# Kernel optimization log

Measured on AMD Instinct MI355X. Metric: run time of the kernel, lower is better.

Reference implementation:

```python
import jax, jax.numpy as jnp
import numpy as np

IMG_W, IMG_H = 800, 800
OH, OW = 7, 7


def setup_inputs() -> dict:
    key = jax.random.key(0)
    k1, k2, k3 = jax.random.split(key, 3)
    feature_map = jax.random.normal(k1, (1, 256, 200, 200), dtype=jnp.float32)
    # boxes in image pixel coords, x1<=x2 and y1<=y2
    xs = jnp.sort(jax.random.uniform(k2, (1024, 2), dtype=jnp.float32) * (IMG_W - 1), axis=1)
    ys = jnp.sort(jax.random.uniform(k3, (1024, 2), dtype=jnp.float32) * (IMG_H - 1), axis=1)
    boxes = jnp.stack([xs[:, 0], ys[:, 0], xs[:, 1], ys[:, 1]], axis=1)
    return {"feature_map": feature_map, "boxes": boxes}


def reference(feature_map, boxes):
    # feature_map: [1, C, H, W]; boxes: [N, 4] (x1, y1, x2, y2) in image coords
    fm = feature_map[0]                      # [C, H, W]
    C, H, W = fm.shape
    scale = jnp.array([W / IMG_W, H / IMG_H, W / IMG_W, H / IMG_H], dtype=boxes.dtype)
    b = jnp.floor(boxes * scale).astype(jnp.int32)
    x1 = jnp.clip(b[:, 0], 0, W - 1)
    y1 = jnp.clip(b[:, 1], 0, H - 1)
    x2 = jnp.clip(b[:, 2] + 1, x1 + 1, W)    # exclusive end, clamped like torch slicing
    y2 = jnp.clip(b[:, 3] + 1, y1 + 1, H)
    rh = y2 - y1                             # [N]
    rw = x2 - x1
    # adaptive_avg_pool2d bin edges: start=floor(i*L/O), end=ceil((i+1)*L/O)
    i = jnp.arange(OH)
    j = jnp.arange(OW)
    rs = y1[:, None] + (i[None, :] * rh[:, None]) // OH                  # [N, OH]
    re = y1[:, None] + ((i[None, :] + 1) * rh[:, None] + OH - 1) // OH
    cs = x1[:, None] + (j[None, :] * rw[:, None]) // OW                  # [N, OW]
    ce = x1[:, None] + ((j[None, :] + 1) * rw[:, None] + OW - 1) // OW
    # integral image with zero row/col padding: ii[c, r, k] = sum fm[c, :r, :k]
    ii = jnp.pad(jnp.cumsum(jnp.cumsum(fm, axis=1), axis=2), ((0, 0), (1, 0), (1, 0)))

    def S(r, c):  # r: [N, OH], c: [N, OW] -> [N, C, OH, OW]
        return ii[:, r[:, :, None], c[:, None, :]].transpose(1, 0, 2, 3)

    total = S(re, ce) - S(rs, ce) - S(re, cs) + S(rs, cs)               # [N, C, OH, OW]
    area = ((re - rs)[:, :, None] * (ce - cs)[:, None, :]).astype(fm.dtype)  # [N, OH, OW]
    return total / area[:, None, :, :]
```

## Files before the change

### kernel.cpp

```cpp
#include <hip/hip_runtime.h>

#define C_CH  256
#define H_FM  200
#define W_FM  200
#define N_BOX 1024
#define OHp   7
#define OWp   7
#define NG    8
#define CG    32
#define WC    (W_FM * C_CH)
#define NCHUNK 25
#define CHROWS 8
#define GSTRIDE (H_FM * W_FM * CG)
#define HSTRIDE (W_FM * CG)
#define AUXG    (NCHUNK * HSTRIDE)
#define GPAD  33


__global__ __launch_bounds__(256) void transpose_wscan_kernel(const float* __restrict__ fm,
                                                              float* __restrict__ T2) {
    __shared__ float tile[W_FM][CG + 1];
    __shared__ float tot[8][CG + 1];
    __shared__ float offE[8][CG + 1];
    const int t = threadIdx.x;
    const int h = blockIdx.x;
    const int g = blockIdx.y;
    const int c0 = g * CG;

    #pragma unroll
    for (int s = 0; s < 25; ++s) {
        int flat = s * 256 + t;
        int ci = flat / W_FM;
        int w  = flat - ci * W_FM;
        tile[w][ci] = fm[(size_t)(c0 + ci) * (H_FM * W_FM) + (size_t)h * W_FM + w];
    }
    __syncthreads();

    const int cg  = t & 31;
    const int chb = t >> 5;
    {
        float acc = 0.0f;
        #pragma unroll
        for (int s = 0; s < 25; ++s) {
            acc += tile[chb * 25 + s][cg];
            tile[chb * 25 + s][cg] = acc;
        }
        tot[chb][cg] = acc;
    }
    __syncthreads();

    {
        float off = 0.0f;
        #pragma unroll
        for (int k = 0; k < 8; ++k) {
            float v = tot[k][cg];
            if (k < chb) off += v;
        }
        offE[chb][cg] = off;
    }
    __syncthreads();

    float* dst = T2 + (size_t)g * GSTRIDE + (size_t)h * HSTRIDE;
    #pragma unroll
    for (int it = 0; it < 7; ++it) {
        int f4 = it * 256 + t;
        if (f4 < 1600) {
            int w  = f4 >> 3;
            int cc = (f4 & 7) * 4;
            int wb = w / 25;
            float4 v;
            v.x = tile[w][cc + 0] + offE[wb][cc + 0];
            v.y = tile[w][cc + 1] + offE[wb][cc + 1];
            v.z = tile[w][cc + 2] + offE[wb][cc + 2];
            v.w = tile[w][cc + 3] + offE[wb][cc + 3];
            *(float4*)(dst + (size_t)f4 * 4) = v;
        }
    }
}

__global__ __launch_bounds__(256) void colscan_chunk_kernel(float* __restrict__ T2,
                                                            float* __restrict__ aux2) {
    const int q4 = blockIdx.x * 256 + threadIdx.x;
    const int ch = blockIdx.y;
    const int g  = q4 / (HSTRIDE / 4);
    const int r4 = q4 - g * (HSTRIDE / 4);
    float4* p = (float4*)T2 + (size_t)g * (GSTRIDE / 4)
                            + (size_t)(ch * CHROWS) * (HSTRIDE / 4) + r4;
    float4 acc = make_float4(0.f, 0.f, 0.f, 0.f);
    #pragma unroll
    for (int k = 0; k < CHROWS; ++k) {
        float4 v = p[(size_t)k * (HSTRIDE / 4)];
        acc.x += v.x; acc.y += v.y; acc.z += v.z; acc.w += v.w;
        p[(size_t)k * (HSTRIDE / 4)] = acc;
    }
    ((float4*)aux2)[(size_t)g * (AUXG / 4) + (size_t)ch * (HSTRIDE / 4) + r4] = acc;
}

__global__ __launch_bounds__(64) void aux_scan_kernel(float* __restrict__ aux2) {
    const int idx = blockIdx.x * 64 + threadIdx.x;
    const int g   = idx / (HSTRIDE / 4);
    const int r4  = idx - g * (HSTRIDE / 4);
    float4* p = (float4*)aux2 + (size_t)g * (AUXG / 4) + r4;
    float4 acc = make_float4(0.f, 0.f, 0.f, 0.f);
    #pragma unroll
    for (int ch = 0; ch < NCHUNK; ++ch) {
        float4 v = p[(size_t)ch * (HSTRIDE / 4)];
        p[(size_t)ch * (HSTRIDE / 4)] = acc;
        acc.x += v.x; acc.y += v.y; acc.z += v.z; acc.w += v.w;
    }
}

__global__ __launch_bounds__(256) void pool8_kernel(const float* __restrict__ T2,
                                                    const float* __restrict__ aux2,
                                                    const float* __restrict__ boxes,
                                                    float* __restrict__ out) {
    __shared__ float grid[196][GPAD];
    __shared__ int er[14];
    __shared__ int ec[14];
    __shared__ float rcpA[49];
    const int bx = blockIdx.x;
    const int n  = bx >> 3;
    const int g  = bx & 7;
    const int t  = threadIdx.x;

    const float4 box = ((const float4*)boxes)[n];
    int b0 = (int)floorf(box.x * 0.25f);
    int b1 = (int)floorf(box.y * 0.25f);
    int b2 = (int)floorf(box.z * 0.25f);
    int b3 = (int)floorf(box.w * 0.25f);
    int x1 = min(max(b0, 0), W_FM - 1);
    int y1 = min(max(b1, 0), H_FM - 1);
    int x2 = min(max(b2 + 1, x1 + 1), W_FM);
    int y2 = min(max(b3 + 1, y1 + 1), H_FM);
    int rh = y2 - y1;
    int rw = x2 - x1;

    if (t < 14) {
        er[t] = (t < 7) ? (y1 + (t * rh) / OHp)
                        : (y1 + ((t - 6) * rh + OHp - 1) / OHp);
    } else if (t >= 64 && t < 78) {
        int u = t - 64;
        ec[u] = (u < 7) ? (x1 + (u * rw) / OWp)
                        : (x1 + ((u - 6) * rw + OWp - 1) / OWp);
    }
    __syncthreads();

    if (t < 49) {
        int i = t / 7;
        int j = t - i * 7;
        rcpA[t] = 1.0f / (float)((er[7 + i] - er[i]) * (ec[7 + j] - ec[j]));
    }

    {
        const int c4 = t & 7;
        const int p0 = t >> 3;
        const float* Tg = T2   + (size_t)g * GSTRIDE + c4 * 4;
        const float* Ag = aux2 + (size_t)g * AUXG   + c4 * 4;
        #pragma unroll
        for (int it = 0; it < 7; ++it) {
            int pos = it * 32 + p0;
            if (pos < 196) {
                int ri = pos / 14;
                int ci = pos - ri * 14;
                int r = er[ri];
                int k = ec[ci];
                float4 v = make_float4(0.f, 0.f, 0.f, 0.f);
                if (r > 0 && k > 0) {
                    float4 tv = *(const float4*)(Tg + ((size_t)(r - 1) * W_FM + (k - 1)) * CG);
                    float4 av = *(const float4*)(Ag + ((size_t)((r - 1) >> 3) * W_FM + (k - 1)) * CG);
                    v.x = tv.x + av.x; v.y = tv.y + av.y;
                    v.z = tv.z + av.z; v.w = tv.w + av.w;
                }
                grid[pos][c4 * 4 + 0] = v.x;
                grid[pos][c4 * 4 + 1] = v.y;
                grid[pos][c4 * 4 + 2] = v.z;
                grid[pos][c4 * 4 + 3] = v.w;
            }
        }
    }
    __syncthreads();

    float* dst = out + (size_t)n * (C_CH * 49) + (size_t)g * (CG * 49);
    #pragma unroll
    for (int k = 0; k < 7; ++k) {
        int flat = k * 256 + t;
        if (flat < CG * 49) {
            int cg  = flat / 49;
            int rem = flat - cg * 49;
            int i = rem / 7;
            int j = rem - i * 7;
            float a = grid[(7 + i) * 14 + 7 + j][cg];
            float b = grid[i * 14 + 7 + j][cg];
            float c = grid[(7 + i) * 14 + j][cg];
            float d = grid[i * 14 + j][cg];
            dst[flat] = ((a - b) - (c - d)) * rcpA[rem];
        }
    }
}

__device__ __forceinline__ void box_edges(const float4 box, int i, int j,
                                          int& rs, int& re, int& cs, int& ce) {
    int b0 = (int)floorf(box.x * 0.25f);
    int b1 = (int)floorf(box.y * 0.25f);
    int b2 = (int)floorf(box.z * 0.25f);
    int b3 = (int)floorf(box.w * 0.25f);
    int x1 = min(max(b0, 0), W_FM - 1);
    int y1 = min(max(b1, 0), H_FM - 1);
    int x2 = min(max(b2 + 1, x1 + 1), W_FM);
    int y2 = min(max(b3 + 1, y1 + 1), H_FM);
    int rh = y2 - y1;
    int rw = x2 - x1;
    rs = y1 + (i * rh) / OHp;
    re = y1 + ((i + 1) * rh + OHp - 1) / OHp;
    cs = x1 + (j * rw) / OWp;
    ce = x1 + ((j + 1) * rw + OWp - 1) / OWp;
}

__global__ __launch_bounds__(256) void pool_direct_kernel(const float* __restrict__ fm,
                                                          const float* __restrict__ boxes,
                                                          float* __restrict__ out) {
    const int idx = blockIdx.x * 256 + threadIdx.x;
    const int j  = idx % OWp;
    const int t1 = idx / OWp;
    const int i  = t1 % OHp;
    const int t2 = t1 / OHp;
    const int c  = t2 % C_CH;
    const int n  = t2 / C_CH;

    const float4 box = ((const float4*)boxes)[n];
    int rs, re, cs, ce;
    box_edges(box, i, j, rs, re, cs, ce);

    const float* base = fm + (size_t)c * (H_FM * W_FM);
    float sum = 0.0f;
    for (int r = rs; r < re; ++r) {
        const float* rowp = base + (size_t)r * W_FM;
        for (int k = cs; k < ce; ++k) sum += rowp[k];
    }
    float area = (float)((re - rs) * (ce - cs));
    out[idx] = sum / area;
}

extern "C" void kernel_launch(void* const* d_in, const int* in_sizes, int n_in,
                              void* d_out, int out_size, void* d_ws, size_t ws_size,
                              hipStream_t stream) {
    const float* fm    = (const float*)d_in[0];
    const float* boxes = (const float*)d_in[1];
    float* out = (float*)d_out;

    const size_t tBytes   = (size_t)NG * GSTRIDE * sizeof(float);
    const size_t auxBytes = (size_t)NG * AUXG * sizeof(float);
    const int    total    = N_BOX * C_CH * OHp * OWp;
    const int    blocks   = total / 256;

    if (ws_size >= tBytes + auxBytes) {
        float* T2   = (float*)d_ws;
        float* aux2 = (float*)((char*)d_ws + tBytes);
        transpose_wscan_kernel<<<dim3(H_FM, NG), 256, 0, stream>>>(fm, T2);
        colscan_chunk_kernel<<<dim3(WC / 4 / 256, NCHUNK), 256, 0, stream>>>(T2, aux2);
        aux_scan_kernel<<<WC / 4 / 64, 64, 0, stream>>>(aux2);
        pool8_kernel<<<N_BOX * NG, 256, 0, stream>>>(T2, aux2, boxes, out);
    } else {
        pool_direct_kernel<<<blocks, 256, 0, stream>>>(fm, boxes, out);
    }
}
```

Baseline: 141.5 us.

## Fuse transpose, row scan and chunked column scan into one kernel

```diff
diff --git a/kernel.cpp b/kernel.cpp
--- a/kernel.cpp
+++ b/kernel.cpp
@@ -8,6 +8,7 @@
 #define OWp   7
 #define NG    8
 #define CG    32
+#define CGP   33
 #define WC    (W_FM * C_CH)
 #define NCHUNK 25
 #define CHROWS 8
@@ -15,85 +16,84 @@
 #define HSTRIDE (W_FM * CG)
 #define AUXG    (NCHUNK * HSTRIDE)
 #define GPAD  33
-
-
-__global__ __launch_bounds__(256) void transpose_wscan_kernel(const float* __restrict__ fm,
-                                                              float* __restrict__ T2) {
-    __shared__ float tile[W_FM][CG + 1];
-    __shared__ float tot[8][CG + 1];
-    __shared__ float offE[8][CG + 1];
-    const int t = threadIdx.x;
-    const int h = blockIdx.x;
-    const int g = blockIdx.y;
-    const int c0 = g * CG;
-
-    #pragma unroll
-    for (int s = 0; s < 25; ++s) {
-        int flat = s * 256 + t;
-        int ci = flat / W_FM;
-        int w  = flat - ci * W_FM;
-        tile[w][ci] = fm[(size_t)(c0 + ci) * (H_FM * W_FM) + (size_t)h * W_FM + w];
-    }
-    __syncthreads();
-
-    const int cg  = t & 31;
-    const int chb = t >> 5;
-    {
-        float acc = 0.0f;
-        #pragma unroll
-        for (int s = 0; s < 25; ++s) {
-            acc += tile[chb * 25 + s][cg];
-            tile[chb * 25 + s][cg] = acc;
-        }
-        tot[chb][cg] = acc;
-    }
-    __syncthreads();
-
-    {
-        float off = 0.0f;
-        #pragma unroll
-        for (int k = 0; k < 8; ++k) {
-            float v = tot[k][cg];
-            if (k < chb) off += v;
-        }
-        offE[chb][cg] = off;
-    }
-    __syncthreads();
-
-    float* dst = T2 + (size_t)g * GSTRIDE + (size_t)h * HSTRIDE;
-    #pragma unroll
-    for (int it = 0; it < 7; ++it) {
-        int f4 = it * 256 + t;
-        if (f4 < 1600) {
-            int w  = f4 >> 3;
-            int cc = (f4 & 7) * 4;
-            int wb = w / 25;
-            float4 v;
-            v.x = tile[w][cc + 0] + offE[wb][cc + 0];
-            v.y = tile[w][cc + 1] + offE[wb][cc + 1];
-            v.z = tile[w][cc + 2] + offE[wb][cc + 2];
-            v.w = tile[w][cc + 3] + offE[wb][cc + 3];
-            *(float4*)(dst + (size_t)f4 * 4) = v;
-        }
-    }
-}
-
-__global__ __launch_bounds__(256) void colscan_chunk_kernel(float* __restrict__ T2,
-                                                            float* __restrict__ aux2) {
-    const int q4 = blockIdx.x * 256 + threadIdx.x;
-    const int ch = blockIdx.y;
-    const int g  = q4 / (HSTRIDE / 4);
-    const int r4 = q4 - g * (HSTRIDE / 4);
-    float4* p = (float4*)T2 + (size_t)g * (GSTRIDE / 4)
-                            + (size_t)(ch * CHROWS) * (HSTRIDE / 4) + r4;
-    float4 acc = make_float4(0.f, 0.f, 0.f, 0.f);
-    #pragma unroll
-    for (int k = 0; k < CHROWS; ++k) {
-        float4 v = p[(size_t)k * (HSTRIDE / 4)];
-        acc.x += v.x; acc.y += v.y; acc.z += v.z; acc.w += v.w;
-        p[(size_t)k * (HSTRIDE / 4)] = acc;
-    }
-    ((float4*)aux2)[(size_t)g * (AUXG / 4) + (size_t)ch * (HSTRIDE / 4) + r4] = acc;
+#define TW    40
+#define NWT   5
+
+
+__global__ __launch_bounds__(256) void fused_scan_kernel(const float* __restrict__ fm,
+                                                         float* __restrict__ T2,
+                                                         float* __restrict__ aux2) {
+    __shared__ float tile[CHROWS][TW][CGP];
+    const int t  = threadIdx.x;
+    const int ch = blockIdx.x;
+    const int g  = blockIdx.y;
+    const int h0 = ch * CHROWS;
+    const float* fmg = fm + (size_t)(g * CG) * (H_FM * W_FM) + (size_t)h0 * W_FM;
+
+    const float* gp[10];
+    int lo[10];
+    #pragma unroll
+    for (int s = 0; s < 10; ++s) {
+        int f   = s * 256 + t;
+        int ci  = f / 80;
+        int rem = f - ci * 80;
+        int r   = rem / 10;
+        int w4  = rem - r * 10;
+        gp[s] = fmg + (size_t)ci * (H_FM * W_FM) + r * W_FM + w4 * 4;
+        lo[s] = (r * TW + w4 * 4) * CGP + ci;
+    }
+
+    const int cg = t & 31;
+    const int rr = t >> 5;
+    float accw = 0.0f;
+    float4 stage[10];
+
+    #pragma unroll
+    for (int s = 0; s < 10; ++s) stage[s] = *(const float4*)(gp[s]);
+
+    for (int wt = 0; wt < NWT; ++wt) {
+        #pragma unroll
+        for (int s = 0; s < 10; ++s) {
+            float4 v = stage[s];
+            float* p = &tile[0][0][0] + lo[s];
+            p[0]       = v.x;
+            p[CGP]     = v.y;
+            p[2 * CGP] = v.z;
+            p[3 * CGP] = v.w;
+        }
+        __syncthreads();
+
+        if (wt + 1 < NWT) {
+            #pragma unroll
+            for (int s = 0; s < 10; ++s)
+                stage[s] = *(const float4*)(gp[s] + (wt + 1) * TW);
+        }
+
+        #pragma unroll
+        for (int w = 0; w < TW; ++w) {
+            accw += tile[rr][w][cg];
+            tile[rr][w][cg] = accw;
+        }
+        __syncthreads();
+
+        float* dstT = T2 + (size_t)g * GSTRIDE;
+        float* dstA = aux2 + (size_t)g * AUXG + (size_t)ch * HSTRIDE;
+        #pragma unroll
+        for (int k = 0; k < 5; ++k) {
+            int col = k * 256 + t;
+            int w   = col >> 5;
+            int cc  = col & 31;
+            float vacc = 0.0f;
+            float* dcol = dstT + (size_t)(wt * TW + w) * CG + cc;
+            #pragma unroll
+            for (int r = 0; r < CHROWS; ++r) {
+                vacc += tile[r][w][cc];
+                dcol[(size_t)(h0 + r) * HSTRIDE] = vacc;
+            }
+            dstA[(size_t)(wt * TW + w) * CG + cc] = vacc;
+        }
+        __syncthreads();
+    }
 }
 
 __global__ __launch_bounds__(64) void aux_scan_kernel(float* __restrict__ aux2) {
@@ -256,8 +256,7 @@
     if (ws_size >= tBytes + auxBytes) {
         float* T2   = (float*)d_ws;
         float* aux2 = (float*)((char*)d_ws + tBytes);
-        transpose_wscan_kernel<<<dim3(H_FM, NG), 256, 0, stream>>>(fm, T2);
-        colscan_chunk_kernel<<<dim3(WC / 4 / 256, NCHUNK), 256, 0, stream>>>(T2, aux2);
+        fused_scan_kernel<<<dim3(NCHUNK, NG), 256, 0, stream>>>(fm, T2, aux2);
         aux_scan_kernel<<<WC / 4 / 64, 64, 0, stream>>>(aux2);
         pool8_kernel<<<N_BOX * NG, 256, 0, stream>>>(T2, aux2, boxes, out);
     } else {
```

Result: faster. 136.5 us (-3.5%).
